# Kernel tuning notes

Measured on AMD Instinct MI355X. Metric: run time of the kernel, lower is better.

The kernel has to match this reference:

```python
import jax, jax.numpy as jnp
import numpy as np

# Loihi neuron constants (from netParams['neuron'])
VTH_MANT = 80.0
THETA = VTH_MANT * 64.0          # Loihi threshold = vThMant * 2**6
I_DECAY = 1024.0                 # current decay (of 4096)
V_DECAY = 128.0                  # voltage decay (of 4096)
REF_DELAY = 1.0                  # refractory steps after a spike
W_SCALE = 64.0                   # Loihi weighted-input scaling (2**6)
TAU_RHO = 1.0
POOL_W = 1.1 * VTH_MANT          # slayer pool synapse weight (one spike fires output)


@jax.custom_vjp
def spike(v):
    return (v >= THETA).astype(v.dtype)

def _spike_fwd(v):
    return spike(v), v

def _spike_bwd(v, g):
    # SLAYER surrogate gradient: exponential pdf around threshold
    return (g * jnp.exp(-jnp.abs(v - THETA) / (TAU_RHO * THETA)) / THETA,)

spike.defvjp(_spike_fwd, _spike_bwd)


def loihi_dynamics(wsum):
    """CUBA Loihi LIF over time-leading weighted input wsum: [T, ...] -> spikes [T, ...]."""
    i_dec = (4096.0 - I_DECAY) / 4096.0
    v_dec = (4096.0 - V_DECAY) / 4096.0

    def step(carry, x):
        u, v, ref = carry
        u = i_dec * u + W_SCALE * x                    # synaptic current
        v = jnp.where(ref > 0, 0.0, v_dec * v + u)     # membrane, clamped in refractory
        s = spike(v)
        v = v * (1.0 - s)                              # reset on spike
        ref = jnp.where(s > 0, REF_DELAY, jnp.maximum(ref - 1.0, 0.0))
        return (u, v, ref), s

    z = jnp.zeros_like(wsum[0])
    _, s = jax.lax.scan(step, (z, z, z), wsum)
    return s


def delay_shift(s):
    # slayer.delayShift(spike, 1): shift spike train by 1 timestep (time-leading axis)
    return jnp.concatenate([jnp.zeros_like(s[:1]), s[:-1]], axis=0)


def conv2d_t(x, w, pad):
    # x: [T, B, C, H, W]; fold T into batch for the spatial conv
    T, B, C, H, W = x.shape
    y = jax.lax.conv_general_dilated(
        x.reshape(T * B, C, H, W), w, (1, 1), [(pad, pad), (pad, pad)],
        dimension_numbers=('NCHW', 'OIHW', 'NCHW'))
    return y.reshape(T, B, y.shape[1], y.shape[2], y.shape[3])


def sum_pool(x, k):
    # slayer pool: per-channel sum pooling with fixed synaptic weight POOL_W
    y = jax.lax.reduce_window(x, 0.0, jax.lax.add,
                              (1, 1, 1, k, k), (1, 1, 1, k, k), 'VALID')
    return POOL_W * y


def setup_inputs() -> dict:
    key = jax.random.key(0)
    ks = jax.random.split(key, 6)
    B, C, H, W, T = 48, 4, 26, 26, 128
    # Bernoulli(0.1) spike trains
    spike_input = (jax.random.uniform(ks[0], (B, C, H, W, T)) < 0.1).astype(jnp.float32)
    w_conv1 = jax.random.normal(ks[1], (8, 4, 5, 5), jnp.float32) * 4.0
    w_conv2 = jax.random.normal(ks[2], (16, 8, 3, 3), jnp.float32) * 4.0
    w_conv3 = jax.random.normal(ks[3], (32, 16, 3, 3), jnp.float32) * 4.0
    w_fc1 = jax.random.normal(ks[4], (512, 3 * 3 * 32), jnp.float32) * 4.0
    w_fc2 = jax.random.normal(ks[5], (2, 512), jnp.float32) * 4.0
    return {"spike_input": spike_input, "w_conv1": w_conv1, "w_conv2": w_conv2,
            "w_conv3": w_conv3, "w_fc1": w_fc1, "w_fc2": w_fc2}


def reference(spike_input, w_conv1, w_conv2, w_conv3, w_fc1, w_fc2):
    x = jnp.transpose(spike_input, (4, 0, 1, 2, 3))  # [T, B, C, H, W]

    def block(x, w, pad):
        s = delay_shift(loihi_dynamics(conv2d_t(x, w, pad)))
        s = delay_shift(loihi_dynamics(sum_pool(s, 2)))
        return s  # dropout is identity in eval

    x = block(x, w_conv1, 1)   # 26 -> 24 -> 12
    x = block(x, w_conv2, 1)   # 12 -> 12 -> 6
    x = block(x, w_conv3, 1)   # 6 -> 6 -> 3
    T, B = x.shape[0], x.shape[1]
    x = x.reshape(T, B, -1)    # [T, B, 32*3*3] (C,H,W flatten order matches torch view)
    s = delay_shift(loihi_dynamics(jnp.einsum('tbi,oi->tbo', x, w_fc1)))
    s = delay_shift(loihi_dynamics(jnp.einsum('tbi,oi->tbo', s, w_fc2)))
    return jnp.transpose(s, (1, 2, 0))  # [B, 2, T]
```

## Files before the change

### kernel.cpp

```cpp
#include <hip/hip_runtime.h>


#define THETA 5120.0f

typedef __attribute__((ext_vector_type(8))) short bfrag;
typedef __attribute__((ext_vector_type(4))) float ffrag;

__device__ __forceinline__ float dyn_step(float x, float& u, float& v, float& r) {
#pragma clang fp contract(off)
    u = 0.75f * u + 64.0f * x;
    float vn = 0.96875f * v + u;
    vn = (r > 0.0f) ? 0.0f : vn;
    float s;
    if (vn >= THETA) { s = 1.0f; v = 0.0f; r = 1.0f; }
    else             { s = 0.0f; v = vn; r = fmaxf(r - 1.0f, 0.0f); }
    return s;
}

__device__ __forceinline__ float dpp_add_xor1(float x) {
    int y = __builtin_amdgcn_update_dpp(0, __float_as_int(x), 0xB1, 0xF, 0xF, true);
    return x + __int_as_float(y);
}
__device__ __forceinline__ float dpp_add_xor2(float x) {
    int y = __builtin_amdgcn_update_dpp(0, __float_as_int(x), 0x4E, 0xF, 0xF, true);
    return x + __int_as_float(y);
}

__device__ __forceinline__ unsigned int compress4(unsigned long long x) {
    x &= 0x1111111111111111ull;
    x = (x | (x >> 3))  & 0x0303030303030303ull;
    x = (x | (x >> 6))  & 0x000F000F000F000Full;
    x = (x | (x >> 12)) & 0x000000FF000000FFull;
    x = (x | (x >> 24)) & 0xFFFFull;
    return (unsigned int)x;
}

__device__ __forceinline__ unsigned short f2bf(float f) {
    unsigned int u = __float_as_uint(f);
    unsigned int r = (u + 0x7FFFu + ((u >> 16) & 1u)) >> 16;
    return (unsigned short)r;
}
__device__ __forceinline__ float bf2f(unsigned short b) {
    return __uint_as_float(((unsigned int)b) << 16);
}

__device__ __forceinline__ float f4_elem(float4 v, int j) {
    return (j == 0) ? v.x : (j == 1) ? v.y : (j == 2) ? v.z : v.w;
}

__global__ __launch_bounds__(256) void k_masks(const float* __restrict__ in,
                                               uint2* __restrict__ xb) {
    int wv = blockIdx.x * 4 + (threadIdx.x >> 6);
    int lane = threadIdx.x & 63;
    int y = wv % 26; int r = wv / 26;
    int pr = r & 1; int b = r >> 1;
    int ch = lane >> 5;
    int x = lane & 31;
    int act = x < 26;
    int xc = act ? x : 25;
    const float4* src = (const float4*)(in + (size_t)(((b * 4 + pr * 2 + ch) * 26 + y) * 26 + xc) * 128);
    uint2* dst = xb + ((size_t)b * 2 + pr) * 28 + (y + 1);
    for (int t4 = 0; t4 < 32; ++t4) {
        float4 f = src[t4];
#pragma unroll
        for (int k = 0; k < 4; ++k) {
            float fv = f4_elem(f, k);
            unsigned long long bal = __ballot(act && (fv != 0.0f));
            if (lane == 0) {
                unsigned int lo = ((unsigned int)bal & 0x03FFFFFFu) << 1;
                unsigned int hi = ((unsigned int)(bal >> 32) & 0x03FFFFFFu) << 1;
                dst[(size_t)(t4 * 4 + k) * 2688] = make_uint2(lo, hi);
            }
        }
    }
}

template<int H>
__global__ __launch_bounds__(576) void k_wsum1(const uint2* __restrict__ xb,
                                               const float* __restrict__ w1,
                                               float* __restrict__ ws) {
    __shared__ float wsh[400];
    __shared__ ffrag tbl4[660];
    int tid = threadIdx.x;
    int tch = blockIdx.x & 15;
    int b = blockIdx.x >> 4;
    if (tid < 400) wsh[tid] = w1[H * 400 + tid];
    __syncthreads();
    for (int e = tid; e < 660; e += 576) {
        int ch = e / 165;
        int rem = e % 165;
        int ky = rem / 33;
        int idx = rem % 33;
        ffrag val = {0.f, 0.f, 0.f, 0.f};
#pragma unroll
        for (int oc4 = 0; oc4 < 4; ++oc4) {
            float a = 0.f;
#pragma unroll
            for (int k = 0; k < 5; ++k)
                a += ((idx >> k) & 1) ? wsh[oc4 * 100 + ch * 25 + ky * 5 + k] : 0.f;
            val[oc4] = a;
        }
        tbl4[(ch * 5 + ky) * 33 + idx] = val;
    }
    __syncthreads();
    int q = tid >> 2, s = tid & 3;
    int ox = (q % 12) * 2 + (s & 1);
    int oy = (q / 12) * 2 + (s >> 1);
    int t0 = tch * 8;
    ffrag acc[8];
#pragma unroll
    for (int j = 0; j < 8; ++j) {
        int t = t0 + j;
        const uint2* rp = xb + ((size_t)t * 48 + b) * 56 + oy;
        ffrag a = {0.f, 0.f, 0.f, 0.f};
#pragma unroll
        for (int ky = 0; ky < 5; ++ky) {
            uint2 r0 = rp[ky];
            uint2 r1 = rp[28 + ky];
            a += tbl4[ky * 33 + (int)((r0.x >> ox) & 31u)];
            a += tbl4[(5 + ky) * 33 + (int)((r0.y >> ox) & 31u)];
            a += tbl4[(10 + ky) * 33 + (int)((r1.x >> ox) & 31u)];
            a += tbl4[(15 + ky) * 33 + (int)((r1.y >> ox) & 31u)];
        }
        acc[j] = a;
    }
    size_t tilebase = (size_t)(t0 >> 4) * 1769472 + (t0 & 15);
#pragma unroll
    for (int oc4 = 0; oc4 < 4; ++oc4) {
        float* wp = ws + tilebase + (size_t)((b * 4 + oc4) * 576 + tid) * 16;
        *(float4*)(wp)     = make_float4(acc[0][oc4], acc[1][oc4], acc[2][oc4], acc[3][oc4]);
        *(float4*)(wp + 4) = make_float4(acc[4][oc4], acc[5][oc4], acc[6][oc4], acc[7][oc4]);
    }
}

template<int H>
__global__ __launch_bounds__(256) void k_scan1(const float* __restrict__ ws,
                                               unsigned short* __restrict__ st1) {
    int wv = blockIdx.x * 4 + (threadIdx.x >> 6);
    int lane = threadIdx.x & 63;
    const float* bp = ws + (size_t)(wv * 64 + lane) * 16;
    unsigned short* so = st1 + ((size_t)(H * 1728 + wv)) * 128;
    float u = 0.f, v = 0.f, rf = 0.f;
    float pu = 0.f, pv = 0.f, prf = 0.f;
    float sp = 0.f;
    unsigned int mb[4];
    float4 cur[4], nxt[4];
#pragma unroll
    for (int i = 0; i < 4; ++i) cur[i] = *(const float4*)(bp + i * 4);
    for (int tb = 0; tb < 8; ++tb) {
        if (tb < 7) {
            const float* np = bp + (size_t)(tb + 1) * 1769472;
#pragma unroll
            for (int i = 0; i < 4; ++i) nxt[i] = *(const float4*)(np + i * 4);
        }
#pragma unroll
        for (int j = 0; j < 16; ++j) {
            int t = tb * 16 + j;
            float w = f4_elem(cur[j >> 2], j & 3);
            float cnt = dpp_add_xor2(dpp_add_xor1(sp));
            float ps = dyn_step(88.0f * cnt, pu, pv, prf);
            unsigned long long bal = __ballot(((lane & 3) == 0) && (ps > 0.5f));
            unsigned int m = compress4(bal);
            int sl = (t >> 1) & 3;
            mb[sl] = (t & 1) ? (mb[sl] | (m << 16)) : m;
            if ((t & 7) == 7 && lane == 0)
                *(uint4*)(so + (t & ~7)) = make_uint4(mb[0], mb[1], mb[2], mb[3]);
            sp = dyn_step(w, u, v, rf);
        }
        if (tb < 7) {
#pragma unroll
            for (int i = 0; i < 4; ++i) cur[i] = nxt[i];
        }
    }
}

__global__ __launch_bounds__(256) void k_mb1(const unsigned short* __restrict__ st1,
                                             unsigned short* __restrict__ pb16) {
    int gid = blockIdx.x * 256 + threadIdx.x;
    int oc = gid & 7; int r = gid >> 3;
    int y = r % 12; r /= 12;
    int b = r % 48; int t = r / 48;
    int base = (oc >> 2) * 1728 + (b * 4 + (oc & 3)) * 9;
    int Q0 = y * 12;
    int w0 = Q0 >> 4, off = Q0 & 15;
    unsigned int v0 = st1[(size_t)(base + w0) * 128 + t];
    unsigned int v1 = (off > 4) ? (unsigned int)st1[(size_t)(base + w0 + 1) * 128 + t] : 0u;
    unsigned int m = ((v0 >> off) | (v1 << (16 - off))) & 0xFFFu;
    pb16[((size_t)(t * 48 + b) * 14 + y + 1) * 8 + oc] = (unsigned short)(m << 1);
}

__global__ __launch_bounds__(576) void k_wsum2(const unsigned short* __restrict__ pb16,
                                               const float* __restrict__ w2,
                                               float* __restrict__ ws) {
    __shared__ float wsh[288];
    __shared__ float tbl[3408];
    int tid = threadIdx.x;
    int tch = blockIdx.x & 3;
    int g = blockIdx.x >> 2;
    if (tid < 288) {
        int oc = (g * 4 + tid / 72) & 15;
        wsh[tid] = w2[oc * 72 + (tid % 72)];
    }
    __syncthreads();
    for (int e = tid; e < 3072; e += 576) {
        int isel = e / 768;
        int pr = (e / 192) % 4;
        int ky = (e / 64) % 3;
        int i = e & 63;
        int lo = i & 7, hi = i >> 3;
        float val = 0.f;
#pragma unroll
        for (int k = 0; k < 3; ++k)
            val += ((lo >> k) & 1) ? wsh[isel * 72 + (2 * pr) * 9 + ky * 3 + k] : 0.f;
#pragma unroll
        for (int k = 0; k < 3; ++k)
            val += ((hi >> k) & 1) ? wsh[isel * 72 + (2 * pr + 1) * 9 + ky * 3 + k] : 0.f;
        tbl[isel * 852 + (pr * 3 + ky) * 71 + lo + 9 * hi] = val;
    }
    __syncthreads();
    int isel = tid / 144;
    int pix = tid % 144;
    int q = pix >> 2, s = pix & 3;
    int ox = (q % 6) * 2 + (s & 1);
    int oy = (q / 6) * 2 + (s >> 1);
    int b = (g * 4 + isel) >> 4;
    const float* tb = tbl + isel * 852;
    float* op = ws + (size_t)(g * 576 + tid) * 16;
    for (int sub = 0; sub < 4; ++sub) {
        int t0 = tch * 32 + sub * 8;
        float acc[8];
#pragma unroll
        for (int j = 0; j < 8; ++j) {
            int t = t0 + j;
            float a = 0.f;
            if (t > 0) {
                const uint4* rp = (const uint4*)(pb16 + (((size_t)(t - 1) * 48 + b) * 14 + oy) * 8);
#pragma unroll
                for (int ky = 0; ky < 3; ++ky) {
                    uint4 row = rp[ky];
                    unsigned int wd[4] = {row.x, row.y, row.z, row.w};
#pragma unroll
                    for (int pr = 0; pr < 4; ++pr) {
                        unsigned int lo = (wd[pr] >> ox) & 7u;
                        unsigned int hi = (wd[pr] >> (16 + ox)) & 7u;
                        a += tb[(pr * 3 + ky) * 71 + (int)(lo + 9u * hi)];
                    }
                }
            }
            acc[j] = a;
        }
        float* wp = op + (size_t)(t0 >> 4) * 1769472 + (t0 & 15);
        *(float4*)(wp)     = make_float4(acc[0], acc[1], acc[2], acc[3]);
        *(float4*)(wp + 4) = make_float4(acc[4], acc[5], acc[6], acc[7]);
    }
}

__global__ __launch_bounds__(576) void k_scan2(const float* __restrict__ ws,
                                               unsigned short* __restrict__ st2) {
    int tid = threadIdx.x;
    int wloc = tid >> 6, lane = tid & 63;
    int g4 = blockIdx.x;
    const float* bp = ws + (size_t)(g4 * 576 + tid) * 16;
    unsigned short* so = st2 + ((size_t)(g4 * 9 + wloc)) * 128;
    float u = 0.f, v = 0.f, rf = 0.f;
    float pu = 0.f, pv = 0.f, prf = 0.f;
    float sp = 0.f;
    unsigned int mb[4];
    float4 cur[4], nxt[4];
#pragma unroll
    for (int i = 0; i < 4; ++i) cur[i] = *(const float4*)(bp + i * 4);
    for (int tb = 0; tb < 8; ++tb) {
        if (tb < 7) {
            const float* np = bp + (size_t)(tb + 1) * 1769472;
#pragma unroll
            for (int i = 0; i < 4; ++i) nxt[i] = *(const float4*)(np + i * 4);
        }
#pragma unroll
        for (int j = 0; j < 16; ++j) {
            int t = tb * 16 + j;
            float w = f4_elem(cur[j >> 2], j & 3);
            float cnt = dpp_add_xor2(dpp_add_xor1(sp));
            float ps = dyn_step(88.0f * cnt, pu, pv, prf);
            unsigned long long bal = __ballot(((lane & 3) == 0) && (ps > 0.5f));
            unsigned int m = compress4(bal);
            int sl = (t >> 1) & 3;
            mb[sl] = (t & 1) ? (mb[sl] | (m << 16)) : m;
            if ((t & 7) == 7 && lane == 0)
                *(uint4*)(so + (t & ~7)) = make_uint4(mb[0], mb[1], mb[2], mb[3]);
            sp = dyn_step(w, u, v, rf);
        }
        if (tb < 7) {
#pragma unroll
            for (int i = 0; i < 4; ++i) cur[i] = nxt[i];
        }
    }
}

__global__ __launch_bounds__(256) void k_mb2(const unsigned short* __restrict__ st2,
                                             unsigned short* __restrict__ pb2) {
    int gid = blockIdx.x * 256 + threadIdx.x;
    int oc = gid & 15; int r = gid >> 4;
    int y = r % 6; r /= 6;
    int b = r % 48; int t = r / 48;
    int img = b * 16 + oc;
    int g4 = img >> 2, lI = img & 3;
    int Q0 = lI * 36 + y * 6;
    int w0 = Q0 >> 4, off = Q0 & 15;
    unsigned int v0 = st2[(size_t)(g4 * 9 + w0) * 128 + t];
    unsigned int v1 = (off > 10) ? (unsigned int)st2[(size_t)(g4 * 9 + w0 + 1) * 128 + t] : 0u;
    unsigned int m = ((v0 >> off) | (v1 << (16 - off))) & 0x3Fu;
    pb2[((size_t)(t * 48 + b) * 8 + y + 1) * 16 + oc] = (unsigned short)(m << 1);
}

__global__ __launch_bounds__(576) void k_wsum3(const unsigned short* __restrict__ pb2,
                                               const float* __restrict__ w3,
                                               float* __restrict__ ws) {
    __shared__ float wsh[576];
    __shared__ float tbl[6816];
    int tid = threadIdx.x;
    int tch = blockIdx.x & 7;
    int gb = blockIdx.x >> 3;
    int ocg = gb / 12, bg = gb % 12;
    {
        int oc_t = ocg * 4 + tid / 144;
        wsh[tid] = w3[oc_t * 144 + (tid % 144)];
    }
    __syncthreads();
    for (int e = tid; e < 6144; e += 576) {
        int osel = e / 1536;
        int pr = (e / 192) % 8;
        int ky = (e / 64) % 3;
        int i = e & 63;
        int lo = i & 7, hi = i >> 3;
        float val = 0.f;
#pragma unroll
        for (int k = 0; k < 3; ++k)
            val += ((lo >> k) & 1) ? wsh[osel * 144 + (2 * pr) * 9 + ky * 3 + k] : 0.f;
#pragma unroll
        for (int k = 0; k < 3; ++k)
            val += ((hi >> k) & 1) ? wsh[osel * 144 + (2 * pr + 1) * 9 + ky * 3 + k] : 0.f;
        tbl[osel * 1704 + (pr * 3 + ky) * 71 + lo + 9 * hi] = val;
    }
    __syncthreads();
    int osel = tid / 144;
    int rem = tid % 144;
    int bsel = rem / 36;
    int pix = rem % 36;
    int q = pix >> 2, s = pix & 3;
    int ox = (q % 3) * 2 + (s & 1);
    int oy = (q / 3) * 2 + (s >> 1);
    int oc = ocg * 4 + osel;
    int b = bg * 4 + bsel;
    const float* tb = tbl + osel * 1704;
    float* op = ws + (size_t)tch * 884736 + (size_t)((b * 32 + oc) * 36 + pix) * 16;
    for (int sub = 0; sub < 2; ++sub) {
        int t0 = tch * 16 + sub * 8;
        float acc[8];
#pragma unroll
        for (int j = 0; j < 8; ++j) {
            int t = t0 + j;
            float a = 0.f;
            if (t > 0) {
                const uint4* rp = (const uint4*)(pb2 + (((size_t)(t - 1) * 48 + b) * 8 + oy) * 16);
#pragma unroll
                for (int ky = 0; ky < 3; ++ky) {
                    uint4 rA = rp[ky * 2];
                    uint4 rB = rp[ky * 2 + 1];
                    unsigned int wd[8] = {rA.x, rA.y, rA.z, rA.w, rB.x, rB.y, rB.z, rB.w};
#pragma unroll
                    for (int pr = 0; pr < 8; ++pr) {
                        unsigned int lo = (wd[pr] >> ox) & 7u;
                        unsigned int hi = (wd[pr] >> (16 + ox)) & 7u;
                        a += tb[(pr * 3 + ky) * 71 + (int)(lo + 9u * hi)];
                    }
                }
            }
            acc[j] = a;
        }
        float* wp = op + sub * 8;
        *(float4*)(wp)     = make_float4(acc[0], acc[1], acc[2], acc[3]);
        *(float4*)(wp + 4) = make_float4(acc[4], acc[5], acc[6], acc[7]);
    }
}

__global__ __launch_bounds__(256) void k_scan3(const float* __restrict__ ws,
                                               unsigned short* __restrict__ st3) {
    int wv = blockIdx.x * 4 + (threadIdx.x >> 6);
    int lane = threadIdx.x & 63;
    const float* bp = ws + (size_t)(wv * 64 + lane) * 16;
    unsigned short* so = st3 + (size_t)wv * 128;
    float u = 0.f, v = 0.f, rf = 0.f;
    float pu = 0.f, pv = 0.f, prf = 0.f;
    float sp = 0.f;
    unsigned int mb[4];
    float4 cur[4], nxt[4];
#pragma unroll
    for (int i = 0; i < 4; ++i) cur[i] = *(const float4*)(bp + i * 4);
    for (int tb = 0; tb < 8; ++tb) {
        if (tb < 7) {
            const float* np = bp + (size_t)(tb + 1) * 884736;
#pragma unroll
            for (int i = 0; i < 4; ++i) nxt[i] = *(const float4*)(np + i * 4);
        }
#pragma unroll
        for (int j = 0; j < 16; ++j) {
            int t = tb * 16 + j;
            float w = f4_elem(cur[j >> 2], j & 3);
            float cnt = dpp_add_xor2(dpp_add_xor1(sp));
            float ps = dyn_step(88.0f * cnt, pu, pv, prf);
            unsigned long long bal = __ballot(((lane & 3) == 0) && (ps > 0.5f));
            unsigned int m = compress4(bal);
            int sl = (t >> 1) & 3;
            mb[sl] = (t & 1) ? (mb[sl] | (m << 16)) : m;
            if ((t & 7) == 7 && lane == 0)
                *(uint4*)(so + (t & ~7)) = make_uint4(mb[0], mb[1], mb[2], mb[3]);
            sp = dyn_step(w, u, v, rf);
        }
        if (tb < 7) {
#pragma unroll
            for (int i = 0; i < 4; ++i) cur[i] = nxt[i];
        }
    }
}

__global__ __launch_bounds__(256) void k_mb3(const unsigned short* __restrict__ st3,
                                             unsigned short* __restrict__ a3) {
    int gid = blockIdx.x * 256 + threadIdx.x;
    if (gid >= 1755648) return;
    int G = gid % 13824, t = gid / 13824;
    unsigned int bit = ((unsigned int)st3[(size_t)(G >> 4) * 128 + t] >> (G & 15)) & 1u;
    a3[(size_t)(t + 1) * 13824 + G] = bit ? 0x3F80 : 0;
}

__global__ __launch_bounds__(256) void k_wsplit(const float* __restrict__ wfc1,
                                                unsigned short* __restrict__ wb) {
    int gid = blockIdx.x * 256 + threadIdx.x;
    int o = gid / 288, k = gid % 288;
    float w = wfc1[gid];
    unsigned short b0 = f2bf(w);
    float r1 = w - bf2f(b0);
    unsigned short b1 = f2bf(r1);
    float r2 = r1 - bf2f(b1);
    unsigned short b2 = f2bf(r2);
    wb[(size_t)k * 512 + o] = b0;
    wb[(size_t)147456 + k * 512 + o] = b1;
    wb[(size_t)294912 + k * 512 + o] = b2;
}

__global__ __launch_bounds__(256) void k_fc1mm(const unsigned short* __restrict__ a3,
                                               const unsigned short* __restrict__ wb,
                                               float* __restrict__ wsf1) {
    __shared__ unsigned short Bs[16 * 872];
    int tid = threadIdx.x;
    int nt = blockIdx.x & 31;
    int mc = blockIdx.x >> 5;
    int n0 = nt * 16;
    for (int idx = tid; idx < 13824; idx += 256) {
        int kp = idx >> 4;
        int n = idx & 15;
        Bs[n * 872 + kp] = wb[(size_t)kp * 512 + n0 + n];
    }
    __syncthreads();
    int wave = tid >> 6;
    int lane = tid & 63;
    int ln = lane & 15, quad = lane >> 4;
#pragma unroll
    for (int i = 0; i < 4; ++i) {
        int m0 = (mc * 16 + wave * 4 + i) * 16;
        const unsigned short* arow = a3 + (size_t)(m0 + ln) * 288 + quad * 8;
        ffrag acc = {0.f, 0.f, 0.f, 0.f};
#pragma unroll
        for (int kb = 0; kb < 9; ++kb) {
            bfrag av = *(const bfrag*)(arow + kb * 32);
#pragma unroll
            for (int c = 0; c < 3; ++c) {
                bfrag bv = *(const bfrag*)(&Bs[ln * 872 + c * 288 + kb * 32 + quad * 8]);
                acc = __builtin_amdgcn_mfma_f32_16x16x32_bf16(av, bv, acc, 0, 0, 0);
            }
        }
        float* wout = wsf1 + (size_t)(m0 + quad * 4) * 512 + n0 + ln;
        wout[0] = acc[0];
        wout[512] = acc[1];
        wout[1024] = acc[2];
        wout[1536] = acc[3];
    }
}

__global__ __launch_bounds__(256) void k_fc1s(const float* __restrict__ wsf1,
                                              float* __restrict__ f1f) {
    int tid = blockIdx.x * 256 + threadIdx.x;
    float u = 0.f, v = 0.f, rf = 0.f;
    float wbuf[16];
#pragma unroll
    for (int i = 0; i < 16; ++i) wbuf[i] = wsf1[(size_t)i * 24576 + tid];
    for (int tb = 0; tb < 128; tb += 16) {
#pragma unroll
        for (int j = 0; j < 16; ++j) {
            int t = tb + j;
            float w = wbuf[j];
            if (t + 16 < 128) wbuf[j] = wsf1[(size_t)(t + 16) * 24576 + tid];
            float s = dyn_step(w, u, v, rf);
            f1f[(size_t)t * 24576 + tid] = s;
        }
    }
}

__global__ __launch_bounds__(256) void k_fc2w(const float* __restrict__ f1f,
                                              const float* __restrict__ wfc2,
                                              float* __restrict__ wsf2) {
    int wv = blockIdx.x * 4 + (threadIdx.x >> 6);
    int lane = threadIdx.x & 63;
    int b = wv % 48, t = wv / 48;
    int o = lane & 1, kq = lane >> 1;
    float acc = 0.f;
    if (t > 0) {
        const float* wp = wfc2 + o * 512 + kq * 16;
        const float* sp = f1f + (size_t)(t - 1) * 24576 + b * 512 + kq * 16;
#pragma unroll
        for (int i = 0; i < 16; ++i) acc += wp[i] * sp[i];
    }
#pragma unroll
    for (int m = 2; m < 64; m <<= 1) acc += __shfl_xor(acc, m, 64);
    if (lane < 2) wsf2[(size_t)t * 96 + b * 2 + o] = acc;
}

__global__ __launch_bounds__(128) void k_fc2s(const float* __restrict__ wsf2,
                                              float* __restrict__ out) {
    int tid = threadIdx.x;
    if (tid >= 96) return;
    float* ob = out + tid * 128;
    ob[0] = 0.0f;
    float u = 0.f, v = 0.f, rf = 0.f;
    float wbuf[8];
#pragma unroll
    for (int i = 0; i < 8; ++i) wbuf[i] = wsf2[(size_t)i * 96 + tid];
    for (int tb = 0; tb < 128; tb += 8) {
#pragma unroll
        for (int j = 0; j < 8; ++j) {
            int t = tb + j;
            float w = wbuf[j];
            if (t + 8 < 128) wbuf[j] = wsf2[(size_t)(t + 8) * 96 + tid];
            float s = dyn_step(w, u, v, rf);
            if (t < 127) ob[t + 1] = s;
        }
    }
}

extern "C" void kernel_launch(void* const* d_in, const int* in_sizes, int n_in,
                              void* d_out, int out_size, void* d_ws, size_t ws_size,
                              hipStream_t stream) {
    const float* in   = (const float*)d_in[0];
    const float* w1   = (const float*)d_in[1];
    const float* w2   = (const float*)d_in[2];
    const float* w3   = (const float*)d_in[3];
    const float* wfc1 = (const float*)d_in[4];
    const float* wfc2 = (const float*)d_in[5];
    float* out = (float*)d_out;
    char* ws = (char*)d_ws;

    float*          slab = (float*)(ws);
    uint2*          xb   = (uint2*)(ws + 56623104);
    unsigned short* pb16 = (unsigned short*)(ws + 59375616);
    unsigned short* pb2  = (unsigned short*)(ws + 60751872);
    float*          f1f  = (float*)(ws + 64094208);
    unsigned short* a3   = (unsigned short*)(ws + 76677120);
    unsigned short* wb   = (unsigned short*)(ws + 80216064);
    unsigned short* st1  = (unsigned short*)(ws + 81100800);
    unsigned short* st2  = (unsigned short*)(ws + 81985536);
    unsigned short* st3  = (unsigned short*)(ws + 82427904);
    float*          wsf1 = (float*)(ws);
    float*          wsf2 = (float*)(ws + 16777216);

    hipMemsetAsync(xb, 0, 2752512, stream);
    hipMemsetAsync(pb16, 0, 1376256, stream);
    hipMemsetAsync(pb2, 0, 1572864, stream);
    hipMemsetAsync(a3, 0, 27648, stream);

    k_wsplit  <<<576, 256, 0, stream>>>(wfc1, wb);
    k_masks   <<<624, 256, 0, stream>>>(in, xb);
    k_wsum1<0><<<768, 576, 0, stream>>>(xb, w1, slab);
    k_scan1<0><<<432, 256, 0, stream>>>(slab, st1);
    k_wsum1<1><<<768, 576, 0, stream>>>(xb, w1, slab);
    k_scan1<1><<<432, 256, 0, stream>>>(slab, st1);
    k_mb1     <<<2304, 256, 0, stream>>>(st1, pb16);
    k_wsum2   <<<768, 576, 0, stream>>>(pb16, w2, slab);
    k_scan2   <<<192, 576, 0, stream>>>(slab, st2);
    k_mb2     <<<2304, 256, 0, stream>>>(st2, pb2);
    k_wsum3   <<<768, 576, 0, stream>>>(pb2, w3, slab);
    k_scan3   <<<216, 256, 0, stream>>>(slab, st3);
    k_mb3     <<<6858, 256, 0, stream>>>(st3, a3);
    k_fc1mm   <<<768, 256, 0, stream>>>(a3, wb, wsf1);
    k_fc1s    <<<96, 256, 0, stream>>>(wsf1, f1f);
    k_fc2w    <<<1536, 256, 0, stream>>>(f1f, wfc2, wsf2);
    k_fc2s    <<<1, 128, 0, stream>>>(wsf2, out);
}
```

Before: 435.3 us.

## Vectorize conv2 lookup table over four output channels per thread

Rebuilds the conv2 weighted-sum lookup table so each entry holds a float4 covering four output channels, and reassigns threads so each handles one pixel for all four channels over eight timesteps, not one channel over thirty-two. One pb16 row load and bit extraction now feeds four channel accumulations, cutting redundant global reads and index math. The cost is wider LDS reads, more accumulator registers (32 floats), and scattered per-channel stores.

```diff
diff --git a/kernel.cpp b/kernel.cpp
--- a/kernel.cpp
+++ b/kernel.cpp
@@ -193,65 +193,68 @@
                                                const float* __restrict__ w2,
                                                float* __restrict__ ws) {
     __shared__ float wsh[288];
-    __shared__ float tbl[3408];
+    __shared__ ffrag tbl4[852];
     int tid = threadIdx.x;
     int tch = blockIdx.x & 3;
-    int g = blockIdx.x >> 2;
-    if (tid < 288) {
-        int oc = (g * 4 + tid / 72) & 15;
-        wsh[tid] = w2[oc * 72 + (tid % 72)];
-    }
-    __syncthreads();
-    for (int e = tid; e < 3072; e += 576) {
-        int isel = e / 768;
-        int pr = (e / 192) % 4;
-        int ky = (e / 64) % 3;
-        int i = e & 63;
-        int lo = i & 7, hi = i >> 3;
-        float val = 0.f;
-#pragma unroll
-        for (int k = 0; k < 3; ++k)
-            val += ((lo >> k) & 1) ? wsh[isel * 72 + (2 * pr) * 9 + ky * 3 + k] : 0.f;
-#pragma unroll
-        for (int k = 0; k < 3; ++k)
-            val += ((hi >> k) & 1) ? wsh[isel * 72 + (2 * pr + 1) * 9 + ky * 3 + k] : 0.f;
-        tbl[isel * 852 + (pr * 3 + ky) * 71 + lo + 9 * hi] = val;
-    }
-    __syncthreads();
-    int isel = tid / 144;
+    int r = blockIdx.x >> 2;
+    int ocg = r & 3; int b = r >> 2;
+    if (tid < 288) wsh[tid] = w2[(ocg * 4 + tid / 72) * 72 + (tid % 72)];
+    __syncthreads();
+    for (int e = tid; e < 852; e += 576) {
+        int pr = e / 213;
+        int rem = e % 213;
+        int ky = rem / 71;
+        int idx = rem % 71;
+        int lo = idx % 9, hi = idx / 9;
+        ffrag val = {0.f, 0.f, 0.f, 0.f};
+#pragma unroll
+        for (int oc4 = 0; oc4 < 4; ++oc4) {
+            float a = 0.f;
+#pragma unroll
+            for (int k = 0; k < 3; ++k)
+                a += ((lo >> k) & 1) ? wsh[oc4 * 72 + (2 * pr) * 9 + ky * 3 + k] : 0.f;
+#pragma unroll
+            for (int k = 0; k < 3; ++k)
+                a += ((hi >> k) & 1) ? wsh[oc4 * 72 + (2 * pr + 1) * 9 + ky * 3 + k] : 0.f;
+            val[oc4] = a;
+        }
+        tbl4[(pr * 3 + ky) * 71 + idx] = val;
+    }
+    __syncthreads();
+    int tq = tid / 144;
     int pix = tid % 144;
     int q = pix >> 2, s = pix & 3;
     int ox = (q % 6) * 2 + (s & 1);
     int oy = (q / 6) * 2 + (s >> 1);
-    int b = (g * 4 + isel) >> 4;
-    const float* tb = tbl + isel * 852;
-    float* op = ws + (size_t)(g * 576 + tid) * 16;
-    for (int sub = 0; sub < 4; ++sub) {
-        int t0 = tch * 32 + sub * 8;
-        float acc[8];
-#pragma unroll
-        for (int j = 0; j < 8; ++j) {
-            int t = t0 + j;
-            float a = 0.f;
-            if (t > 0) {
-                const uint4* rp = (const uint4*)(pb16 + (((size_t)(t - 1) * 48 + b) * 14 + oy) * 8);
-#pragma unroll
-                for (int ky = 0; ky < 3; ++ky) {
-                    uint4 row = rp[ky];
-                    unsigned int wd[4] = {row.x, row.y, row.z, row.w};
-#pragma unroll
-                    for (int pr = 0; pr < 4; ++pr) {
-                        unsigned int lo = (wd[pr] >> ox) & 7u;
-                        unsigned int hi = (wd[pr] >> (16 + ox)) & 7u;
-                        a += tb[(pr * 3 + ky) * 71 + (int)(lo + 9u * hi)];
-                    }
+    int t0 = tch * 32 + tq * 8;
+    ffrag acc[8];
+#pragma unroll
+    for (int j = 0; j < 8; ++j) {
+        int t = t0 + j;
+        ffrag a = {0.f, 0.f, 0.f, 0.f};
+        if (t > 0) {
+            const uint4* rp = (const uint4*)(pb16 + (((size_t)(t - 1) * 48 + b) * 14 + oy) * 8);
+#pragma unroll
+            for (int ky = 0; ky < 3; ++ky) {
+                uint4 row = rp[ky];
+                unsigned int wd[4] = {row.x, row.y, row.z, row.w};
+#pragma unroll
+                for (int pr = 0; pr < 4; ++pr) {
+                    unsigned int lo = (wd[pr] >> ox) & 7u;
+                    unsigned int hi = (wd[pr] >> (16 + ox)) & 7u;
+                    a += tbl4[(pr * 3 + ky) * 71 + (int)(lo + 9u * hi)];
                 }
             }
-            acc[j] = a;
-        }
-        float* wp = op + (size_t)(t0 >> 4) * 1769472 + (t0 & 15);
-        *(float4*)(wp)     = make_float4(acc[0], acc[1], acc[2], acc[3]);
-        *(float4*)(wp + 4) = make_float4(acc[4], acc[5], acc[6], acc[7]);
+        }
+        acc[j] = a;
+    }
+    size_t tilebase = (size_t)(t0 >> 4) * 1769472 + (t0 & 15);
+#pragma unroll
+    for (int oc4 = 0; oc4 < 4; ++oc4) {
+        int neuron = (b * 16 + ocg * 4 + oc4) * 144 + pix;
+        float* wp = ws + tilebase + (size_t)neuron * 16;
+        *(float4*)(wp)     = make_float4(acc[0][oc4], acc[1][oc4], acc[2][oc4], acc[3][oc4]);
+        *(float4*)(wp + 4) = make_float4(acc[4][oc4], acc[5][oc4], acc[6][oc4], acc[7][oc4]);
     }
 }
 
```

Result: faster. 418.3 us (-3.9%).
